# Kernel tuning notes

Measured on AMD Instinct MI355X. Metric: run time of the kernel, lower is better.

Reference implementation:

```python
import jax, jax.numpy as jnp
import numpy as np

N = 50000   # nodes
E = 800000  # directed edges
D = 128     # input_channels


def _kaiming(key, shape):
    fan_in = shape[0]
    return jax.random.normal(key, shape, jnp.float32) * np.float32(np.sqrt(2.0 / fan_in))


def setup_inputs():
    key = jax.random.key(0)
    ks = jax.random.split(key, 8)
    x = jax.random.normal(ks[0], (N, D), jnp.float32)
    edge_index = jax.random.randint(ks[1], (2, E), 0, N, dtype=jnp.int32)
    return {
        "x": x,
        "edge_index": edge_index,
        "W_in": _kaiming(ks[2], (D, D)),      "b_in": jnp.zeros((D,), jnp.float32),
        "W1": _kaiming(ks[3], (D, 2 * D)),    "b1": jnp.zeros((2 * D,), jnp.float32),
        "W2": _kaiming(ks[4], (2 * D, D)),    "b2": jnp.zeros((D,), jnp.float32),
        "W3": _kaiming(ks[5], (D, D // 2)),   "b3": jnp.zeros((D // 2,), jnp.float32),
        "W_out": _kaiming(ks[6], (D // 2, 1)), "b_out": jnp.zeros((1,), jnp.float32),
    }


def _gcn_conv(x, src, dst, W, b, n):
    """PyG GCNConv: add self-loops, symmetric D^-1/2 (A+I) D^-1/2 normalization."""
    h = x @ W  # [n, out]
    loop = jnp.arange(n, dtype=src.dtype)
    s = jnp.concatenate([src, loop])  # message sources (x_j)
    d = jnp.concatenate([dst, loop])  # aggregation targets (x_i)
    deg = jax.ops.segment_sum(jnp.ones_like(d, jnp.float32), d, num_segments=n)
    dis = jnp.where(deg > 0, jax.lax.rsqrt(jnp.maximum(deg, 1.0)), 0.0)
    norm = dis[s] * dis[d]  # [E+n]
    msg = h[s] * norm[:, None]  # gather + scale
    out = jax.ops.segment_sum(msg, d, num_segments=n)  # scatter-add
    return out + b


def reference(x, edge_index, W_in, b_in, W1, b1, W2, b2, W3, b3, W_out, b_out):
    src, dst = edge_index[0], edge_index[1]
    n = x.shape[0]
    lrelu = lambda t: jax.nn.leaky_relu(t, 0.01)
    # dropout in eval mode (identity)
    h = lrelu(x @ W_in + b_in)
    h = lrelu(_gcn_conv(h, src, dst, W1, b1, n))
    h = lrelu(_gcn_conv(h, src, dst, W2, b2, n))
    h = lrelu(_gcn_conv(h, src, dst, W3, b3, n))
    return h @ W_out + b_out  # [n, 1]
```

## Files before the change

### kernel.cpp

```cpp
#include <hip/hip_runtime.h>


#define LRELU(v) ((v) > 0.f ? (v) : 0.01f * (v))

typedef __attribute__((ext_vector_type(8))) _Float16 half8;
typedef __attribute__((ext_vector_type(8))) float float8;
typedef __attribute__((ext_vector_type(4))) float floatx4;

constexpr int CAP = 64;

__global__ __launch_bounds__(256) void k_prep(const int* __restrict__ src,
                                              const int* __restrict__ dst,
                                              int* __restrict__ cnt,
                                              unsigned short* __restrict__ pad,
                                              const float* __restrict__ W_in,
                                              const float* __restrict__ W1,
                                              const float* __restrict__ W2,
                                              const float* __restrict__ W3,
                                              _Float16* __restrict__ wt_in,
                                              _Float16* __restrict__ wt1,
                                              _Float16* __restrict__ wt2,
                                              _Float16* __restrict__ wt3,
                                              int E, int PR) {
  const int b = blockIdx.x;
  const int tid = threadIdx.x;
  if (b < 128) {
    const int m = b >> 5;
    const int blk = b & 31;
    const int idx = blk * 256 + tid;
    if (m == 0) {
      for (int i = idx; i < 128 * 128; i += 8192) {
        const int k = i >> 7, f = i & 127;
        wt_in[f * 128 + k] = (_Float16)W_in[i];
      }
    } else if (m == 1) {
      for (int i = idx; i < 128 * 256; i += 8192) {
        const int k = i >> 8, f = i & 255;
        wt1[f * 128 + k] = (_Float16)W1[i];
      }
    } else if (m == 2) {
      for (int i = idx; i < 256 * 128; i += 8192) {
        const int k = i >> 7, f = i & 127;
        wt2[f * 256 + k] = (_Float16)W2[i];
      }
    } else {
      for (int i = idx; i < 128 * 64; i += 8192) {
        const int k = i >> 6, f = i & 63;
        wt3[f * 128 + k] = (_Float16)W3[i];
      }
    }
  } else {
    const int bb = b - 128;
    const int range = bb & 7;
    const int chunk = bb >> 3;
    const int e = chunk * 256 + tid;
    if (e < E) {
      const int d = dst[e];
      if (d / PR == range) {
        const int pos = atomicAdd(&cnt[d], 1);
        if (pos < CAP) pad[(long)d * CAP + pos] = (unsigned short)src[e];
      }
    }
  }
}

template <int K, int F, int EPI, typename IT>
__global__ __launch_bounds__(256) void k_gemm(const IT* __restrict__ X,
                                              const _Float16* __restrict__ Wt,
                                              const float* __restrict__ b,
                                              const int* __restrict__ cnt,
                                              _Float16* __restrict__ out, int M) {
  constexpr int TM = 64;
  constexpr int PAD = 8;
  constexpr int LK = K + PAD;
  constexpr int CW = F / 4;
  constexpr int NT = CW / 16;
  constexpr int NK = K / 32;
  __shared__ _Float16 xs[TM * LK];

  const int m0 = blockIdx.x * TM;
  const int tid = threadIdx.x;
  const int w = tid >> 6;
  const int lane = tid & 63;
  const int m = lane & 15;
  const int q = lane >> 4;

  half8 breg[NT][NK];
#pragma unroll
  for (int t = 0; t < NT; ++t)
#pragma unroll
    for (int kc = 0; kc < NK; ++kc)
      breg[t][kc] =
          *(const half8*)&Wt[(long)(w * CW + t * 16 + m) * K + kc * 32 + q * 8];

  constexpr int CPR = K / 8;
  for (int idx = tid; idx < TM * CPR; idx += 256) {
    const int row = idx / CPR;
    const int kk = idx % CPR;
    const int g = m0 + row;
    half8 h = (half8)(_Float16)0.f;
    if (g < M) {
      if constexpr (sizeof(IT) == 4) {
        const float4* p = (const float4*)&X[(long)g * K + kk * 8];
        float4 a = p[0], c = p[1];
        h[0] = (_Float16)a.x; h[1] = (_Float16)a.y;
        h[2] = (_Float16)a.z; h[3] = (_Float16)a.w;
        h[4] = (_Float16)c.x; h[5] = (_Float16)c.y;
        h[6] = (_Float16)c.z; h[7] = (_Float16)c.w;
      } else {
        h = *(const half8*)&X[(long)g * K + kk * 8];
      }
    }
    *(half8*)&xs[row * LK + kk * 8] = h;
  }
  __syncthreads();

  floatx4 acc[4][NT];
#pragma unroll
  for (int rt = 0; rt < 4; ++rt)
#pragma unroll
    for (int t = 0; t < NT; ++t) acc[rt][t] = (floatx4){0.f, 0.f, 0.f, 0.f};

#pragma unroll
  for (int kc = 0; kc < NK; ++kc) {
    half8 af[4];
#pragma unroll
    for (int rt = 0; rt < 4; ++rt)
      af[rt] = *(const half8*)&xs[(rt * 16 + m) * LK + kc * 32 + q * 8];
#pragma unroll
    for (int rt = 0; rt < 4; ++rt)
#pragma unroll
      for (int t = 0; t < NT; ++t)
        acc[rt][t] = __builtin_amdgcn_mfma_f32_16x16x32_f16(af[rt], breg[t][kc],
                                                            acc[rt][t], 0, 0, 0);
  }

#pragma unroll
  for (int rt = 0; rt < 4; ++rt) {
#pragma unroll
    for (int r = 0; r < 4; ++r) {
      const int row = m0 + rt * 16 + q * 4 + r;
      if (row < M) {
        const float dv = rsqrtf((float)cnt[row] + 1.0f);
#pragma unroll
        for (int t = 0; t < NT; ++t) {
          const int col = w * CW + t * 16 + m;
          float v = acc[rt][t][r];
          if constexpr (EPI == 0) { v += b[col]; v = LRELU(v); v *= dv; }
          if constexpr (EPI == 2) { v *= dv; }
          out[(long)row * F + col] = (_Float16)v;
        }
      }
    }
  }
}

__global__ __launch_bounds__(256) void k_gemm2x(const _Float16* __restrict__ X,
                                                const _Float16* __restrict__ Wt1,
                                                const float* __restrict__ b1,
                                                const _Float16* __restrict__ Wt2,
                                                const int* __restrict__ cnt,
                                                _Float16* __restrict__ out,
                                                int M) {
  constexpr int TM = 64;
  constexpr int LK1 = 128 + 8;
  constexpr int LK2 = 256 + 8;
  __shared__ _Float16 xs[TM * LK1];
  __shared__ _Float16 ys[TM * LK2];

  const int m0 = blockIdx.x * TM;
  const int tid = threadIdx.x;
  const int w = tid >> 6;
  const int lane = tid & 63;
  const int m = lane & 15;
  const int q = lane >> 4;

  for (int idx = tid; idx < TM * 16; idx += 256) {
    const int row = idx >> 4;
    const int kk = idx & 15;
    const int g = m0 + row;
    half8 h = (half8)(_Float16)0.f;
    if (g < M) h = *(const half8*)&X[(long)g * 128 + kk * 8];
    *(half8*)&xs[row * LK1 + kk * 8] = h;
  }

  half8 breg1[4][4];
#pragma unroll
  for (int t = 0; t < 4; ++t)
#pragma unroll
    for (int kc = 0; kc < 4; ++kc)
      breg1[t][kc] =
          *(const half8*)&Wt1[(long)(w * 64 + t * 16 + m) * 128 + kc * 32 + q * 8];

  __syncthreads();

  floatx4 acc1[4][4];
#pragma unroll
  for (int rt = 0; rt < 4; ++rt)
#pragma unroll
    for (int t = 0; t < 4; ++t) acc1[rt][t] = (floatx4){0.f, 0.f, 0.f, 0.f};

#pragma unroll
  for (int kc = 0; kc < 4; ++kc) {
    half8 af[4];
#pragma unroll
    for (int rt = 0; rt < 4; ++rt)
      af[rt] = *(const half8*)&xs[(rt * 16 + m) * LK1 + kc * 32 + q * 8];
#pragma unroll
    for (int rt = 0; rt < 4; ++rt)
#pragma unroll
      for (int t = 0; t < 4; ++t)
        acc1[rt][t] = __builtin_amdgcn_mfma_f32_16x16x32_f16(af[rt], breg1[t][kc],
                                                             acc1[rt][t], 0, 0, 0);
  }

#pragma unroll
  for (int rt = 0; rt < 4; ++rt) {
#pragma unroll
    for (int r = 0; r < 4; ++r) {
      const int row = rt * 16 + q * 4 + r;
#pragma unroll
      for (int t = 0; t < 4; ++t) {
        const int col = w * 64 + t * 16 + m;
        float v = acc1[rt][t][r] + b1[col];
        ys[row * LK2 + col] = (_Float16)LRELU(v);
      }
    }
  }

  half8 breg2[2][8];
#pragma unroll
  for (int t = 0; t < 2; ++t)
#pragma unroll
    for (int kc = 0; kc < 8; ++kc)
      breg2[t][kc] =
          *(const half8*)&Wt2[(long)(w * 32 + t * 16 + m) * 256 + kc * 32 + q * 8];

  __syncthreads();

  floatx4 acc2[4][2];
#pragma unroll
  for (int rt = 0; rt < 4; ++rt)
#pragma unroll
    for (int t = 0; t < 2; ++t) acc2[rt][t] = (floatx4){0.f, 0.f, 0.f, 0.f};

#pragma unroll
  for (int kc = 0; kc < 8; ++kc) {
    half8 af[4];
#pragma unroll
    for (int rt = 0; rt < 4; ++rt)
      af[rt] = *(const half8*)&ys[(rt * 16 + m) * LK2 + kc * 32 + q * 8];
#pragma unroll
    for (int rt = 0; rt < 4; ++rt)
#pragma unroll
      for (int t = 0; t < 2; ++t)
        acc2[rt][t] = __builtin_amdgcn_mfma_f32_16x16x32_f16(af[rt], breg2[t][kc],
                                                             acc2[rt][t], 0, 0, 0);
  }

#pragma unroll
  for (int rt = 0; rt < 4; ++rt) {
#pragma unroll
    for (int r = 0; r < 4; ++r) {
      const int row = m0 + rt * 16 + q * 4 + r;
      if (row < M) {
        const float dv = rsqrtf((float)cnt[row] + 1.0f);
#pragma unroll
        for (int t = 0; t < 2; ++t) {
          const int col = w * 32 + t * 16 + m;
          out[(long)row * 128 + col] = (_Float16)(acc2[rt][t][r] * dv);
        }
      }
    }
  }
}

template <int F, int MODE>
__global__ __launch_bounds__(256) void k_agg(const _Float16* __restrict__ G,
                                             const unsigned short* __restrict__ pad,
                                             const int* __restrict__ cnt,
                                             const float* __restrict__ b,
                                             const float* __restrict__ Wout,
                                             const float* __restrict__ bout,
                                             void* __restrict__ out, int N) {
  const int w = threadIdx.x >> 6;
  const int lane = threadIdx.x & 63;
  const int c = lane & 7;
  const int j = lane >> 3;
  const int n = j >> 2;
  const int jj = j & 3;
  const int i0 = blockIdx.x * 8 + w * 2;
  int i = i0 + n;
  const bool valid = (i < N);
  if (!valid) i = N - 1;
  const int col0 = (F == 128) ? ((int)blockIdx.y << 6) : 0;

  const _Float16* gbase = G + col0 + c * 8;
  const int cn = min(cnt[i], CAP);
  const unsigned short* plist = pad + (long)i * CAP;

  float8 acc = {0.f, 0.f, 0.f, 0.f, 0.f, 0.f, 0.f, 0.f};
  if (jj == 0)
    acc = __builtin_convertvector(*(const half8*)(gbase + (long)i * F), float8);
  for (int e = jj; e < cn; e += 4) {
    const int s = plist[e];
    acc += __builtin_convertvector(*(const half8*)(gbase + (long)s * F), float8);
  }
#pragma unroll
  for (int k = 0; k < 8; ++k) {
    acc[k] += __shfl_xor(acc[k], 8);
    acc[k] += __shfl_xor(acc[k], 16);
  }

  const float dv = rsqrtf((float)cnt[i] + 1.0f);
  if constexpr (MODE == 2) {
    float p = 0.f;
#pragma unroll
    for (int k = 0; k < 8; ++k) {
      const int col = c * 8 + k;
      float v = acc[k] * dv + b[col];
      v = LRELU(v);
      p += v * Wout[col];
    }
    p += __shfl_xor(p, 1);
    p += __shfl_xor(p, 2);
    p += __shfl_xor(p, 4);
    if (valid && jj == 0 && c == 0) ((float*)out)[i] = p + bout[0];
  } else {
    if (valid && jj == 0) {
      half8 hv;
#pragma unroll
      for (int k = 0; k < 8; ++k) {
        float v = acc[k] * dv;
        if constexpr (MODE == 1) { v += b[col0 + c * 8 + k]; v = LRELU(v); }
        hv[k] = (_Float16)v;
      }
      *(half8*)&((_Float16*)out)[(long)i * F + col0 + c * 8] = hv;
    }
  }
}


extern "C" void kernel_launch(void* const* d_in, const int* in_sizes, int n_in,
                              void* d_out, int out_size, void* d_ws, size_t ws_size,
                              hipStream_t stream) {
  const float* x     = (const float*)d_in[0];
  const int* eidx    = (const int*)d_in[1];
  const float* W_in  = (const float*)d_in[2];
  const float* b_in  = (const float*)d_in[3];
  const float* W1    = (const float*)d_in[4];
  const float* b1    = (const float*)d_in[5];
  const float* W2    = (const float*)d_in[6];
  const float* b2    = (const float*)d_in[7];
  const float* W3    = (const float*)d_in[8];
  const float* b3    = (const float*)d_in[9];
  const float* W_out = (const float*)d_in[10];
  const float* b_out = (const float*)d_in[11];
  float* out = (float*)d_out;

  const int N = in_sizes[0] / 128;
  const int E = in_sizes[1] / 2;
  const int* src = eidx;
  const int* dst = eidx + E;
  const int PR = (N + 7) / 8;

  size_t off = 0;
  char* base = (char*)d_ws;
  auto alloc = [&](size_t bytes) -> void* {
    void* p = base + off;
    off = (off + bytes + 255) & ~(size_t)255;
    return p;
  };
  int* cnt            = (int*)alloc((size_t)N * sizeof(int));
  unsigned short* pad = (unsigned short*)alloc((size_t)N * CAP * 2);
  _Float16* wt_in     = (_Float16*)alloc((size_t)128 * 128 * 2);
  _Float16* wt1       = (_Float16*)alloc((size_t)256 * 128 * 2);
  _Float16* wt2       = (_Float16*)alloc((size_t)128 * 256 * 2);
  _Float16* wt3       = (_Float16*)alloc((size_t)64 * 128 * 2);
  _Float16* buf1      = (_Float16*)alloc((size_t)N * 128 * 2);
  _Float16* buf2      = (_Float16*)alloc((size_t)N * 128 * 2);
  _Float16* buf3      = (_Float16*)alloc((size_t)N * 64 * 2);

  hipMemsetAsync(cnt, 0, (size_t)N * sizeof(int), stream);

  const int gE = (E + 255) / 256;
  const int gRows = (N + 63) / 64;
  const int gAggP = (N + 7) / 8;

  k_prep<<<128 + 8 * gE, 256, 0, stream>>>(src, dst, cnt, pad,
                                           W_in, W1, W2, W3,
                                           wt_in, wt1, wt2, wt3, E, PR);

  k_gemm<128, 128, 0, float><<<gRows, 256, 0, stream>>>(x, wt_in, b_in, cnt,
                                                        buf1, N);
  k_agg<128, 0><<<dim3(gAggP, 2), 256, 0, stream>>>(buf1, pad, cnt, nullptr,
                                                    nullptr, nullptr, buf2, N);
  k_gemm2x<<<gRows, 256, 0, stream>>>(buf2, wt1, b1, wt2, cnt, buf1, N);
  k_agg<128, 1><<<dim3(gAggP, 2), 256, 0, stream>>>(buf1, pad, cnt, b2,
                                                    nullptr, nullptr, buf2, N);
  k_gemm<128, 64, 2, _Float16><<<gRows, 256, 0, stream>>>(buf2, wt3, nullptr,
                                                          cnt, buf3, N);
  k_agg<64, 2><<<gAggP, 256, 0, stream>>>(buf3, pad, cnt, b3,
                                          W_out, b_out, out, N);
}
```

Baseline: 273.4 us.

## Fuse input GEMM with CSR build and read fp32 weights directly in GEMMs

Removes the weight-transpose prep pass, so GEMMs load fp32 weights with strided reads and convert them in registers. The input-layer GEMM now runs in the same launch as the edge bucketing, which means the first aggregation has to apply per-source degree normalisation itself (gathering cnt[s] per edge). Aggregation kernels now handle a full 128-wide row per wave with four independent accumulators, replacing the two column-half launches. The dual GEMM also shares one LDS buffer for both stages to cut shared-memory use. The trade-off is strided, uncoalesced weight loads in every GEMM block and an extra gather of cnt per edge in the first aggregation.

```diff
diff --git a/kernel.cpp b/kernel.cpp
--- a/kernel.cpp
+++ b/kernel.cpp
@@ -9,76 +9,30 @@
 
 constexpr int CAP = 64;
 
-__global__ __launch_bounds__(256) void k_prep(const int* __restrict__ src,
-                                              const int* __restrict__ dst,
-                                              int* __restrict__ cnt,
-                                              unsigned short* __restrict__ pad,
-                                              const float* __restrict__ W_in,
-                                              const float* __restrict__ W1,
-                                              const float* __restrict__ W2,
-                                              const float* __restrict__ W3,
-                                              _Float16* __restrict__ wt_in,
-                                              _Float16* __restrict__ wt1,
-                                              _Float16* __restrict__ wt2,
-                                              _Float16* __restrict__ wt3,
-                                              int E, int PR) {
-  const int b = blockIdx.x;
-  const int tid = threadIdx.x;
-  if (b < 128) {
-    const int m = b >> 5;
-    const int blk = b & 31;
-    const int idx = blk * 256 + tid;
-    if (m == 0) {
-      for (int i = idx; i < 128 * 128; i += 8192) {
-        const int k = i >> 7, f = i & 127;
-        wt_in[f * 128 + k] = (_Float16)W_in[i];
-      }
-    } else if (m == 1) {
-      for (int i = idx; i < 128 * 256; i += 8192) {
-        const int k = i >> 8, f = i & 255;
-        wt1[f * 128 + k] = (_Float16)W1[i];
-      }
-    } else if (m == 2) {
-      for (int i = idx; i < 256 * 128; i += 8192) {
-        const int k = i >> 7, f = i & 127;
-        wt2[f * 256 + k] = (_Float16)W2[i];
-      }
-    } else {
-      for (int i = idx; i < 128 * 64; i += 8192) {
-        const int k = i >> 6, f = i & 63;
-        wt3[f * 128 + k] = (_Float16)W3[i];
-      }
-    }
-  } else {
-    const int bb = b - 128;
-    const int range = bb & 7;
-    const int chunk = bb >> 3;
-    const int e = chunk * 256 + tid;
-    if (e < E) {
-      const int d = dst[e];
-      if (d / PR == range) {
-        const int pos = atomicAdd(&cnt[d], 1);
-        if (pos < CAP) pad[(long)d * CAP + pos] = (unsigned short)src[e];
-      }
-    }
-  }
+template <int F>
+__device__ __forceinline__ half8 loadB(const float* __restrict__ W, int k0,
+                                       int col) {
+  half8 h;
+#pragma unroll
+  for (int j = 0; j < 8; ++j) h[j] = (_Float16)W[(long)(k0 + j) * F + col];
+  return h;
 }
 
 template <int K, int F, int EPI, typename IT>
-__global__ __launch_bounds__(256) void k_gemm(const IT* __restrict__ X,
-                                              const _Float16* __restrict__ Wt,
-                                              const float* __restrict__ b,
-                                              const int* __restrict__ cnt,
-                                              _Float16* __restrict__ out, int M) {
+__device__ __forceinline__ void gemm_tile(const IT* __restrict__ X,
+                                          const float* __restrict__ W,
+                                          const float* __restrict__ bias,
+                                          const int* __restrict__ cnt,
+                                          _Float16* __restrict__ out, int M,
+                                          int tile, _Float16* __restrict__ xs) {
   constexpr int TM = 64;
   constexpr int PAD = 8;
   constexpr int LK = K + PAD;
   constexpr int CW = F / 4;
   constexpr int NT = CW / 16;
   constexpr int NK = K / 32;
-  __shared__ _Float16 xs[TM * LK];
-
-  const int m0 = blockIdx.x * TM;
+
+  const int m0 = tile * TM;
   const int tid = threadIdx.x;
   const int w = tid >> 6;
   const int lane = tid & 63;
@@ -90,8 +44,7 @@
   for (int t = 0; t < NT; ++t)
 #pragma unroll
     for (int kc = 0; kc < NK; ++kc)
-      breg[t][kc] =
-          *(const half8*)&Wt[(long)(w * CW + t * 16 + m) * K + kc * 32 + q * 8];
+      breg[t][kc] = loadB<F>(W, kc * 32 + q * 8, w * CW + t * 16 + m);
 
   constexpr int CPR = K / 8;
   for (int idx = tid; idx < TM * CPR; idx += 256) {
@@ -102,11 +55,11 @@
     if (g < M) {
       if constexpr (sizeof(IT) == 4) {
         const float4* p = (const float4*)&X[(long)g * K + kk * 8];
-        float4 a = p[0], c = p[1];
+        float4 a = p[0], cc = p[1];
         h[0] = (_Float16)a.x; h[1] = (_Float16)a.y;
         h[2] = (_Float16)a.z; h[3] = (_Float16)a.w;
-        h[4] = (_Float16)c.x; h[5] = (_Float16)c.y;
-        h[6] = (_Float16)c.z; h[7] = (_Float16)c.w;
+        h[4] = (_Float16)cc.x; h[5] = (_Float16)cc.y;
+        h[6] = (_Float16)cc.z; h[7] = (_Float16)cc.w;
       } else {
         h = *(const half8*)&X[(long)g * K + kk * 8];
       }
@@ -141,12 +94,13 @@
     for (int r = 0; r < 4; ++r) {
       const int row = m0 + rt * 16 + q * 4 + r;
       if (row < M) {
-        const float dv = rsqrtf((float)cnt[row] + 1.0f);
+        float dv = 1.f;
+        if constexpr (EPI == 2) dv = rsqrtf((float)cnt[row] + 1.0f);
 #pragma unroll
         for (int t = 0; t < NT; ++t) {
           const int col = w * CW + t * 16 + m;
           float v = acc[rt][t][r];
-          if constexpr (EPI == 0) { v += b[col]; v = LRELU(v); v *= dv; }
+          if constexpr (EPI == 1) { v += bias[col]; v = LRELU(v); }
           if constexpr (EPI == 2) { v *= dv; }
           out[(long)row * F + col] = (_Float16)v;
         }
@@ -155,27 +109,63 @@
   }
 }
 
-__global__ __launch_bounds__(256) void k_gemm2x(const _Float16* __restrict__ X,
-                                                const _Float16* __restrict__ Wt1,
-                                                const float* __restrict__ b1,
-                                                const _Float16* __restrict__ Wt2,
-                                                const int* __restrict__ cnt,
-                                                _Float16* __restrict__ out,
-                                                int M) {
-  constexpr int TM = 64;
+__global__ __launch_bounds__(256) void k_sg(const float* __restrict__ x,
+                                            const float* __restrict__ W_in,
+                                            const float* __restrict__ b_in,
+                                            const int* __restrict__ src,
+                                            const int* __restrict__ dst,
+                                            int* __restrict__ cnt,
+                                            unsigned short* __restrict__ pad,
+                                            _Float16* __restrict__ h0,
+                                            int N, int E, int PR,
+                                            int gemmBlocks) {
+  __shared__ _Float16 xs[64 * 136];
+  const int b = blockIdx.x;
+  if (b < gemmBlocks) {
+    gemm_tile<128, 128, 1, float>(x, W_in, b_in, nullptr, h0, N, b, xs);
+  } else {
+    const int bb = b - gemmBlocks;
+    const int range = bb & 7;
+    const int e = (bb >> 3) * 256 + (int)threadIdx.x;
+    if (e < E) {
+      const int d = dst[e];
+      if ((unsigned)(d - range * PR) < (unsigned)PR) {
+        const int pos = atomicAdd(&cnt[d], 1);
+        if (pos < CAP) pad[(long)d * CAP + pos] = (unsigned short)src[e];
+      }
+    }
+  }
+}
+
+__global__ __launch_bounds__(256) void k_gemm3(const _Float16* __restrict__ X,
+                                               const float* __restrict__ W3,
+                                               const int* __restrict__ cnt,
+                                               _Float16* __restrict__ out,
+                                               int M) {
+  __shared__ _Float16 xs[64 * 136];
+  gemm_tile<128, 64, 2, _Float16>(X, W3, nullptr, cnt, out, M, blockIdx.x, xs);
+}
+
+__global__ __launch_bounds__(256) void k_g2x(const _Float16* __restrict__ X,
+                                             const float* __restrict__ W1,
+                                             const float* __restrict__ b1,
+                                             const float* __restrict__ W2,
+                                             const int* __restrict__ cnt,
+                                             _Float16* __restrict__ out, int M) {
   constexpr int LK1 = 128 + 8;
   constexpr int LK2 = 256 + 8;
-  __shared__ _Float16 xs[TM * LK1];
-  __shared__ _Float16 ys[TM * LK2];
-
-  const int m0 = blockIdx.x * TM;
+  __shared__ _Float16 smem[64 * LK2];
+  _Float16* xs = smem;
+  _Float16* ys = smem;
+
+  const int m0 = blockIdx.x * 64;
   const int tid = threadIdx.x;
   const int w = tid >> 6;
   const int lane = tid & 63;
   const int m = lane & 15;
   const int q = lane >> 4;
 
-  for (int idx = tid; idx < TM * 16; idx += 256) {
+  for (int idx = tid; idx < 64 * 16; idx += 256) {
     const int row = idx >> 4;
     const int kk = idx & 15;
     const int g = m0 + row;
@@ -189,8 +179,7 @@
   for (int t = 0; t < 4; ++t)
 #pragma unroll
     for (int kc = 0; kc < 4; ++kc)
-      breg1[t][kc] =
-          *(const half8*)&Wt1[(long)(w * 64 + t * 16 + m) * 128 + kc * 32 + q * 8];
+      breg1[t][kc] = loadB<256>(W1, kc * 32 + q * 8, w * 64 + t * 16 + m);
 
   __syncthreads();
 
@@ -213,6 +202,15 @@
         acc1[rt][t] = __builtin_amdgcn_mfma_f32_16x16x32_f16(af[rt], breg1[t][kc],
                                                              acc1[rt][t], 0, 0, 0);
   }
+
+  half8 breg2[2][8];
+#pragma unroll
+  for (int t = 0; t < 2; ++t)
+#pragma unroll
+    for (int kc = 0; kc < 8; ++kc)
+      breg2[t][kc] = loadB<128>(W2, kc * 32 + q * 8, w * 32 + t * 16 + m);
+
+  __syncthreads();
 
 #pragma unroll
   for (int rt = 0; rt < 4; ++rt) {
@@ -228,14 +226,6 @@
     }
   }
 
-  half8 breg2[2][8];
-#pragma unroll
-  for (int t = 0; t < 2; ++t)
-#pragma unroll
-    for (int kc = 0; kc < 8; ++kc)
-      breg2[t][kc] =
-          *(const half8*)&Wt2[(long)(w * 32 + t * 16 + m) * 256 + kc * 32 + q * 8];
-
   __syncthreads();
 
   floatx4 acc2[4][2];
@@ -275,69 +265,176 @@
   }
 }
 
-template <int F, int MODE>
-__global__ __launch_bounds__(256) void k_agg(const _Float16* __restrict__ G,
-                                             const unsigned short* __restrict__ pad,
-                                             const int* __restrict__ cnt,
-                                             const float* __restrict__ b,
-                                             const float* __restrict__ Wout,
-                                             const float* __restrict__ bout,
-                                             void* __restrict__ out, int N) {
+__global__ __launch_bounds__(256) void k_agg_pre(const _Float16* __restrict__ G,
+                                                 const unsigned short* __restrict__ pad,
+                                                 const int* __restrict__ cnt,
+                                                 _Float16* __restrict__ out,
+                                                 int N) {
+  const int w = threadIdx.x >> 6;
+  const int lane = threadIdx.x & 63;
+  const int c = lane & 15;
+  const int jj = lane >> 4;
+  int i = blockIdx.x * 4 + w;
+  const bool valid = (i < N);
+  if (!valid) i = N - 1;
+  const int cni = cnt[i];
+  const int cn = min(cni, CAP);
+  const float dvi = rsqrtf((float)cni + 1.f);
+  const _Float16* gb = G + c * 8;
+  const unsigned short* pl = pad + (long)i * CAP;
+
+  float8 a0 = {0.f, 0.f, 0.f, 0.f, 0.f, 0.f, 0.f, 0.f};
+  float8 a1 = a0, a2 = a0, a3 = a0;
+  if (jj == 0) {
+    float8 f = __builtin_convertvector(*(const half8*)(gb + (long)i * 128), float8);
+#pragma unroll
+    for (int k = 0; k < 8; ++k) a0[k] = f[k] * dvi;
+  }
+  int e = jj;
+  for (; e + 12 < cn; e += 16) {
+    const int s0 = pl[e], s1 = pl[e + 4], s2 = pl[e + 8], s3 = pl[e + 12];
+    const float d0 = rsqrtf((float)cnt[s0] + 1.f);
+    const float d1 = rsqrtf((float)cnt[s1] + 1.f);
+    const float d2 = rsqrtf((float)cnt[s2] + 1.f);
+    const float d3 = rsqrtf((float)cnt[s3] + 1.f);
+    float8 f0 = __builtin_convertvector(*(const half8*)(gb + (long)s0 * 128), float8);
+    float8 f1 = __builtin_convertvector(*(const half8*)(gb + (long)s1 * 128), float8);
+    float8 f2 = __builtin_convertvector(*(const half8*)(gb + (long)s2 * 128), float8);
+    float8 f3 = __builtin_convertvector(*(const half8*)(gb + (long)s3 * 128), float8);
+#pragma unroll
+    for (int k = 0; k < 8; ++k) {
+      a0[k] += f0[k] * d0;
+      a1[k] += f1[k] * d1;
+      a2[k] += f2[k] * d2;
+      a3[k] += f3[k] * d3;
+    }
+  }
+  for (; e < cn; e += 4) {
+    const int s = pl[e];
+    const float d = rsqrtf((float)cnt[s] + 1.f);
+    float8 f = __builtin_convertvector(*(const half8*)(gb + (long)s * 128), float8);
+#pragma unroll
+    for (int k = 0; k < 8; ++k) a0[k] += f[k] * d;
+  }
+#pragma unroll
+  for (int k = 0; k < 8; ++k) a0[k] += a1[k] + a2[k] + a3[k];
+#pragma unroll
+  for (int k = 0; k < 8; ++k) {
+    a0[k] += __shfl_xor(a0[k], 16);
+    a0[k] += __shfl_xor(a0[k], 32);
+  }
+  if (valid && jj == 0) {
+    half8 hv;
+#pragma unroll
+    for (int k = 0; k < 8; ++k) hv[k] = (_Float16)(a0[k] * dvi);
+    *(half8*)&out[(long)i * 128 + c * 8] = hv;
+  }
+}
+
+__global__ __launch_bounds__(256) void k_agg_post(const _Float16* __restrict__ G,
+                                                  const unsigned short* __restrict__ pad,
+                                                  const int* __restrict__ cnt,
+                                                  const float* __restrict__ bias,
+                                                  _Float16* __restrict__ out,
+                                                  int N) {
+  const int w = threadIdx.x >> 6;
+  const int lane = threadIdx.x & 63;
+  const int c = lane & 15;
+  const int jj = lane >> 4;
+  int i = blockIdx.x * 4 + w;
+  const bool valid = (i < N);
+  if (!valid) i = N - 1;
+  const int cni = cnt[i];
+  const int cn = min(cni, CAP);
+  const float dvi = rsqrtf((float)cni + 1.f);
+  const _Float16* gb = G + c * 8;
+  const unsigned short* pl = pad + (long)i * CAP;
+
+  float8 a0 = {0.f, 0.f, 0.f, 0.f, 0.f, 0.f, 0.f, 0.f};
+  float8 a1 = a0, a2 = a0, a3 = a0;
+  if (jj == 0)
+    a0 = __builtin_convertvector(*(const half8*)(gb + (long)i * 128), float8);
+  int e = jj;
+  for (; e + 12 < cn; e += 16) {
+    const int s0 = pl[e], s1 = pl[e + 4], s2 = pl[e + 8], s3 = pl[e + 12];
+    a0 += __builtin_convertvector(*(const half8*)(gb + (long)s0 * 128), float8);
+    a1 += __builtin_convertvector(*(const half8*)(gb + (long)s1 * 128), float8);
+    a2 += __builtin_convertvector(*(const half8*)(gb + (long)s2 * 128), float8);
+    a3 += __builtin_convertvector(*(const half8*)(gb + (long)s3 * 128), float8);
+  }
+  for (; e < cn; e += 4) {
+    const int s = pl[e];
+    a0 += __builtin_convertvector(*(const half8*)(gb + (long)s * 128), float8);
+  }
+  a0 += a1 + a2 + a3;
+#pragma unroll
+  for (int k = 0; k < 8; ++k) {
+    a0[k] += __shfl_xor(a0[k], 16);
+    a0[k] += __shfl_xor(a0[k], 32);
+  }
+  if (valid && jj == 0) {
+    half8 hv;
+#pragma unroll
+    for (int k = 0; k < 8; ++k) {
+      float v = a0[k] * dvi + bias[c * 8 + k];
+      hv[k] = (_Float16)LRELU(v);
+    }
+    *(half8*)&out[(long)i * 128 + c * 8] = hv;
+  }
+}
+
+__global__ __launch_bounds__(256) void k_agg_final(const _Float16* __restrict__ G,
+                                                   const unsigned short* __restrict__ pad,
+                                                   const int* __restrict__ cnt,
+                                                   const float* __restrict__ b3,
+                                                   const float* __restrict__ Wout,
+                                                   const float* __restrict__ bout,
+                                                   float* __restrict__ out, int N) {
   const int w = threadIdx.x >> 6;
   const int lane = threadIdx.x & 63;
   const int c = lane & 7;
   const int j = lane >> 3;
   const int n = j >> 2;
   const int jj = j & 3;
-  const int i0 = blockIdx.x * 8 + w * 2;
-  int i = i0 + n;
+  int i = blockIdx.x * 8 + w * 2 + n;
   const bool valid = (i < N);
   if (!valid) i = N - 1;
-  const int col0 = (F == 128) ? ((int)blockIdx.y << 6) : 0;
-
-  const _Float16* gbase = G + col0 + c * 8;
-  const int cn = min(cnt[i], CAP);
-  const unsigned short* plist = pad + (long)i * CAP;
-
-  float8 acc = {0.f, 0.f, 0.f, 0.f, 0.f, 0.f, 0.f, 0.f};
+  const int cni = cnt[i];
+  const int cn = min(cni, CAP);
+  const float dvi = rsqrtf((float)cni + 1.f);
+  const _Float16* gb = G + c * 8;
+  const unsigned short* pl = pad + (long)i * CAP;
+
+  float8 a0 = {0.f, 0.f, 0.f, 0.f, 0.f, 0.f, 0.f, 0.f};
+  float8 a1 = a0;
   if (jj == 0)
-    acc = __builtin_convertvector(*(const half8*)(gbase + (long)i * F), float8);
-  for (int e = jj; e < cn; e += 4) {
-    const int s = plist[e];
-    acc += __builtin_convertvector(*(const half8*)(gbase + (long)s * F), float8);
-  }
+    a0 = __builtin_convertvector(*(const half8*)(gb + (long)i * 64), float8);
+  int e = jj;
+  for (; e + 4 < cn; e += 8) {
+    const int s0 = pl[e], s1 = pl[e + 4];
+    a0 += __builtin_convertvector(*(const half8*)(gb + (long)s0 * 64), float8);
+    a1 += __builtin_convertvector(*(const half8*)(gb + (long)s1 * 64), float8);
+  }
+  if (e < cn)
+    a0 += __builtin_convertvector(*(const half8*)(gb + (long)pl[e] * 64), float8);
+  a0 += a1;
 #pragma unroll
   for (int k = 0; k < 8; ++k) {
-    acc[k] += __shfl_xor(acc[k], 8);
-    acc[k] += __shfl_xor(acc[k], 16);
-  }
-
-  const float dv = rsqrtf((float)cnt[i] + 1.0f);
-  if constexpr (MODE == 2) {
-    float p = 0.f;
-#pragma unroll
-    for (int k = 0; k < 8; ++k) {
-      const int col = c * 8 + k;
-      float v = acc[k] * dv + b[col];
-      v = LRELU(v);
-      p += v * Wout[col];
-    }
-    p += __shfl_xor(p, 1);
-    p += __shfl_xor(p, 2);
-    p += __shfl_xor(p, 4);
-    if (valid && jj == 0 && c == 0) ((float*)out)[i] = p + bout[0];
-  } else {
-    if (valid && jj == 0) {
-      half8 hv;
-#pragma unroll
-      for (int k = 0; k < 8; ++k) {
-        float v = acc[k] * dv;
-        if constexpr (MODE == 1) { v += b[col0 + c * 8 + k]; v = LRELU(v); }
-        hv[k] = (_Float16)v;
-      }
-      *(half8*)&((_Float16*)out)[(long)i * F + col0 + c * 8] = hv;
-    }
-  }
+    a0[k] += __shfl_xor(a0[k], 8);
+    a0[k] += __shfl_xor(a0[k], 16);
+  }
+  float p = 0.f;
+#pragma unroll
+  for (int k = 0; k < 8; ++k) {
+    const int col = c * 8 + k;
+    float v = a0[k] * dvi + b3[col];
+    v = LRELU(v);
+    p += v * Wout[col];
+  }
+  p += __shfl_xor(p, 1);
+  p += __shfl_xor(p, 2);
+  p += __shfl_xor(p, 4);
+  if (valid && jj == 0 && c == 0) out[i] = p + bout[0];
 }
 
 
@@ -373,33 +470,23 @@
   };
   int* cnt            = (int*)alloc((size_t)N * sizeof(int));
   unsigned short* pad = (unsigned short*)alloc((size_t)N * CAP * 2);
-  _Float16* wt_in     = (_Float16*)alloc((size_t)128 * 128 * 2);
-  _Float16* wt1       = (_Float16*)alloc((size_t)256 * 128 * 2);
-  _Float16* wt2       = (_Float16*)alloc((size_t)128 * 256 * 2);
-  _Float16* wt3       = (_Float16*)alloc((size_t)64 * 128 * 2);
   _Float16* buf1      = (_Float16*)alloc((size_t)N * 128 * 2);
   _Float16* buf2      = (_Float16*)alloc((size_t)N * 128 * 2);
   _Float16* buf3      = (_Float16*)alloc((size_t)N * 64 * 2);
 
   hipMemsetAsync(cnt, 0, (size_t)N * sizeof(int), stream);
 
-  const int gE = (E + 255) / 256;
+  const int gE8 = 8 * ((E + 255) / 256);
   const int gRows = (N + 63) / 64;
-  const int gAggP = (N + 7) / 8;
-
-  k_prep<<<128 + 8 * gE, 256, 0, stream>>>(src, dst, cnt, pad,
-                                           W_in, W1, W2, W3,
-                                           wt_in, wt1, wt2, wt3, E, PR);
-
-  k_gemm<128, 128, 0, float><<<gRows, 256, 0, stream>>>(x, wt_in, b_in, cnt,
-                                                        buf1, N);
-  k_agg<128, 0><<<dim3(gAggP, 2), 256, 0, stream>>>(buf1, pad, cnt, nullptr,
-                                                    nullptr, nullptr, buf2, N);
-  k_gemm2x<<<gRows, 256, 0, stream>>>(buf2, wt1, b1, wt2, cnt, buf1, N);
-  k_agg<128, 1><<<dim3(gAggP, 2), 256, 0, stream>>>(buf1, pad, cnt, b2,
-                                                    nullptr, nullptr, buf2, N);
-  k_gemm<128, 64, 2, _Float16><<<gRows, 256, 0, stream>>>(buf2, wt3, nullptr,
-                                                          cnt, buf3, N);
-  k_agg<64, 2><<<gAggP, 256, 0, stream>>>(buf3, pad, cnt, b3,
-                                          W_out, b_out, out, N);
-}
+  const int gAgg = (N + 3) / 4;
+  const int gAggF = (N + 7) / 8;
+
+  k_sg<<<gRows + gE8, 256, 0, stream>>>(x, W_in, b_in, src, dst, cnt, pad,
+                                        buf1, N, E, PR, gRows);
+  k_agg_pre<<<gAgg, 256, 0, stream>>>(buf1, pad, cnt, buf2, N);
+  k_g2x<<<gRows, 256, 0, stream>>>(buf2, W1, b1, W2, cnt, buf1, N);
+  k_agg_post<<<gAgg, 256, 0, stream>>>(buf1, pad, cnt, b2, buf2, N);
+  k_gemm3<<<gRows, 256, 0, stream>>>(buf2, W3, cnt, buf3, N);
+  k_agg_final<<<gAggF, 256, 0, stream>>>(buf3, pad, cnt, b3, W_out, b_out,
+                                         out, N);
+}
```

Result: slower. 283.8 us (+3.8%).
